# Optimization experiments

Hardware: AMD Instinct MI355X
Metric: run time of the kernel (lower is better)

## Reference

```python
import jax, jax.numpy as jnp
import numpy as np

HEADS = 8
B, N, DIM = 8, 1024, 128  # n must be a perfect square (H=W=32)
LN_EPS = 1e-5


def _region_means(xg):
    """Four-quadrant region means per position via integral image.
    xg: [b,H,W,d] -> [b,H,W,4,d]. For position (h,w) the torch code pools:
      r1 = x[:, :h+1, :w+1], r2 = x[:, :h+1, w:], r3 = x[:, h:, :w+1], r4 = x[:, h:, w:]
    """
    b, H, W, d = xg.shape
    # padded 2D prefix sum: P[:, i, j] = sum over rows<i, cols<j
    P = jnp.pad(jnp.cumsum(jnp.cumsum(xg, axis=1), axis=2),
                ((0, 0), (1, 0), (1, 0), (0, 0)))
    r1 = P[:, 1:, 1:]                                              # sum x[:h+1,:w+1]
    r2 = P[:, 1:, -1:] - P[:, 1:, :-1]                             # sum x[:h+1, w:]
    r3 = P[:, -1:, 1:] - P[:, :-1, 1:]                             # sum x[h:, :w+1]
    r4 = P[:, -1:, -1:] - P[:, :-1, -1:] - P[:, -1:, :-1] + P[:, :-1, :-1]
    ah = jnp.arange(H, dtype=xg.dtype)
    aw = jnp.arange(W, dtype=xg.dtype)
    hp1 = (ah + 1.0)[:, None]   # h+1
    wp1 = (aw + 1.0)[None, :]   # w+1
    hr = (H - ah)[:, None]      # H-h
    wr = (W - aw)[None, :]      # W-w
    c1 = (hp1 * wp1)[None, :, :, None]
    c2 = (hp1 * wr)[None, :, :, None]
    c3 = (hr * wp1)[None, :, :, None]
    c4 = (hr * wr)[None, :, :, None]
    return jnp.stack([r1 / c1, r2 / c2, r3 / c3, r4 / c4], axis=3)


def setup_inputs() -> dict:
    key = jax.random.key(0)
    ks = jax.random.split(key, 10)
    s = 0.02
    return {
        "x": jax.random.normal(ks[0], (B, N, DIM), jnp.float32),
        "ln_g": jnp.ones((DIM,), jnp.float32),
        "ln_b": jnp.zeros((DIM,), jnp.float32),
        "Wqkv": jax.random.normal(ks[1], (DIM, 3 * HEADS * DIM), jnp.float32) * s,
        "bqkv": jax.random.normal(ks[2], (3 * HEADS * DIM,), jnp.float32) * s,
        "Wq": jax.random.normal(ks[3], (DIM, DIM), jnp.float32) * s,
        "Wk": jax.random.normal(ks[4], (DIM, DIM), jnp.float32) * s,
        "Wv": jax.random.normal(ks[5], (DIM, DIM), jnp.float32) * s,
        "Wo": jax.random.normal(ks[6], (DIM, DIM), jnp.float32) * s,
        "bo": jax.random.normal(ks[7], (DIM,), jnp.float32) * s,
        "Wout": jax.random.normal(ks[8], (HEADS * DIM, DIM), jnp.float32) * s,
        "bout": jax.random.normal(ks[9], (DIM,), jnp.float32) * s,
    }


def reference(x, ln_g, ln_b, Wqkv, bqkv, Wq, Wk, Wv, Wo, bo, Wout, bout):
    b, n, dim = x.shape
    H = W = int(n ** 0.5)
    # LayerNorm
    mu = jnp.mean(x, axis=-1, keepdims=True)
    var = jnp.mean(jnp.square(x - mu), axis=-1, keepdims=True)
    xn = (x - mu) * jax.lax.rsqrt(var + LN_EPS) * ln_g + ln_b
    # qkv projection; only q is actually used downstream (k,v chunks are dead)
    qkv = xn @ Wqkv + bqkv
    q = qkv[..., : HEADS * dim].reshape(b, n, HEADS, dim).transpose(0, 2, 1, 3)  # [b,h,n,d]
    # region features, identical across heads -> keep unbroadcast [b,n,4,d]
    regions = _region_means(xn.reshape(b, H, W, dim)).reshape(b, n, 4, dim)
    # RegionAggregator
    qh = q @ Wq                                   # [b,h,n,d]
    k = jnp.einsum('bnrd,de->bnre', regions, Wk)  # [b,n,4,d]
    v = jnp.einsum('bnrd,de->bnre', regions, Wv)
    scale = (dim // HEADS) ** -0.5
    attn = jax.nn.softmax(jnp.einsum('bhnd,bnrd->bhnr', qh, k) * scale, axis=-1)
    agg = jnp.einsum('bhnr,bnrd->bhnd', attn, v)
    out = agg @ Wo + bo                           # [b,h,n,d]
    out = out.transpose(0, 2, 1, 3).reshape(b, n, HEADS * dim)
    return out @ Wout + bout
```

## Files before the change

### kernel.cpp

```cpp
#include <hip/hip_runtime.h>
#include <hip/hip_bf16.h>
#include <stdint.h>

#define HEADS 8
#define NN 1024
#define DIM 128
#define HW 32
#define LN_EPS 1e-5f

typedef __hip_bfloat16 bf16;
typedef __bf16 bf16x8 __attribute__((ext_vector_type(8)));
typedef float floatx4 __attribute__((ext_vector_type(4)));

__device__ __forceinline__ float b2f(bf16 v){ return __bfloat162float(v); }
__device__ __forceinline__ bf16 f2b(float v){ return __float2bfloat16(v); }

__device__ __forceinline__ float ldin(const void* p, size_t i, int f){
    return f ? ((const float*)p)[i] : b2f(((const bf16*)p)[i]);
}
__device__ __forceinline__ float4 ldin4(const void* p, size_t i, int f){
    if (f) return *reinterpret_cast<const float4*>((const float*)p + i);
    ushort4 u = *reinterpret_cast<const ushort4*>((const bf16*)p + i);
    float4 r;
    r.x = b2f(*(bf16*)&u.x); r.y = b2f(*(bf16*)&u.y);
    r.z = b2f(*(bf16*)&u.z); r.w = b2f(*(bf16*)&u.w);
    return r;
}
__device__ __forceinline__ int dtf(const void* g){
    return (((const uint32_t*)g)[0] == 0x3F800000u) ? 1 : 0;
}

__global__ __launch_bounds__(256) void lnscan_kernel(const void* __restrict__ x,
                                                     const void* __restrict__ g,
                                                     const void* __restrict__ bta,
                                                     bf16* __restrict__ xn,
                                                     float* __restrict__ P){
    __shared__ float lnv[32][128];
    int f = dtf(g);
    int b = blockIdx.x >> 5, hh = blockIdx.x & 31;
    int wv = threadIdx.x >> 6, lane = threadIdx.x & 63;
    float gl0 = ldin(g, lane, f),    gl1 = ldin(g, lane+64, f);
    float bl0 = ldin(bta, lane, f),  bl1 = ldin(bta, lane+64, f);
    size_t rowbase = (size_t)b*NN + (size_t)hh*HW;
#pragma unroll
    for (int rnd=0; rnd<8; rnd++){
        int w = rnd*4 + wv;
        size_t base = (rowbase + w)*DIM;
        float v0 = ldin(x, base+lane,    f);
        float v1 = ldin(x, base+lane+64, f);
        float s = v0+v1, ss = v0*v0+v1*v1;
        for (int o=32;o;o>>=1){ s += __shfl_xor(s,o,64); ss += __shfl_xor(ss,o,64); }
        float mu = s * (1.0f/DIM);
        float var = ss * (1.0f/DIM) - mu*mu;
        float rs = rsqrtf(var + LN_EPS);
        float y0 = (v0-mu)*rs*gl0 + bl0;
        float y1 = (v1-mu)*rs*gl1 + bl1;
        xn[base+lane]    = f2b(y0);
        xn[base+lane+64] = f2b(y1);
        lnv[w][lane]    = y0;
        lnv[w][lane+64] = y1;
    }
    __syncthreads();
    if (threadIdx.x < 128){
        int c = threadIdx.x;
        float run = 0.f;
        float* Pr = P + rowbase*DIM + c;
#pragma unroll
        for (int w=0; w<HW; w++){
            run += lnv[w][c];
            Pr[(size_t)w*DIM] = run;
        }
    }
}

__global__ __launch_bounds__(128) void colscan_kernel(float* __restrict__ P){
    int b = blockIdx.x >> 5, w = blockIdx.x & 31, c = threadIdx.x;
    float* Pc = P + ((size_t)(b*NN + w))*DIM + c;
    float run = 0.f;
    for (int h=0; h<HW; h++){
        size_t o = (size_t)h*HW*DIM;
        run += Pc[o]; Pc[o] = run;
    }
}

__global__ __launch_bounds__(256) void prep_kernel(const void* __restrict__ Wqkv,
                                                   const void* __restrict__ bqkv,
                                                   const void* __restrict__ Wq,
                                                   const void* __restrict__ Wk,
                                                   const void* __restrict__ Wv,
                                                   const void* __restrict__ Wo,
                                                   const void* __restrict__ bo,
                                                   const void* __restrict__ Wout,
                                                   const void* __restrict__ ln_g,
                                                   bf16* __restrict__ WhT,
                                                   bf16* __restrict__ WhoT,
                                                   bf16* __restrict__ WkvT,
                                                   float* __restrict__ bq,
                                                   float* __restrict__ bfin_part){
    __shared__ float S1[128][132];
    __shared__ float S2[8][132];
    int f = dtf(ln_g);
    int t = threadIdx.x;
    int blk = blockIdx.x;
    if (blk < 128){
        int h = blk >> 4, dc = blk & 15;
#pragma unroll
        for (int i=0;i<16;i++){
            int idx4 = (t + i*256)*4;
            int k = idx4 >> 7, e = idx4 & 127;
            *reinterpret_cast<float4*>(&S1[k][e]) = ldin4(Wq, idx4, f);
        }
        {
            int idx4 = t*4;
            int dl = idx4 >> 7, k = idx4 & 127;
            *reinterpret_cast<float4*>(&S2[dl][k]) =
                ldin4(Wqkv, (size_t)(dc*8+dl)*3072 + h*128 + k, f);
        }
        __syncthreads();
        int d = t & 7;
        int e0 = (t >> 3) * 4;
        float acc[4] = {0.f,0.f,0.f,0.f};
        for (int k=0;k<128;k++){
            float a = S2[d][k];
            float4 wv = *reinterpret_cast<const float4*>(&S1[k][e0]);
            acc[0] += a*wv.x; acc[1] += a*wv.y; acc[2] += a*wv.z; acc[3] += a*wv.w;
        }
#pragma unroll
        for (int i=0;i<4;i++)
            WhT[(size_t)(h*128 + e0 + i)*128 + dc*8 + d] = f2b(acc[i]);
    } else if (blk < 256){
        int h = (blk-128) >> 4, dc = (blk-128) & 15;
#pragma unroll
        for (int i=0;i<16;i++){
            int idx4 = (t + i*256)*4;
            int k = idx4 >> 7, e = idx4 & 127;
            *reinterpret_cast<float4*>(&S1[k][e]) =
                ldin4(Wout, (size_t)(h*128 + k)*128 + e, f);
        }
        {
            int idx4 = t*4;
            int dl = idx4 >> 7, k = idx4 & 127;
            *reinterpret_cast<float4*>(&S2[dl][k]) =
                ldin4(Wo, (size_t)(dc*8+dl)*128 + k, f);
        }
        __syncthreads();
        int d = t & 7;
        int e0 = (t >> 3) * 4;
        float acc[4] = {0.f,0.f,0.f,0.f};
        for (int k=0;k<128;k++){
            float a = S2[d][k];
            float4 wv = *reinterpret_cast<const float4*>(&S1[k][e0]);
            acc[0] += a*wv.x; acc[1] += a*wv.y; acc[2] += a*wv.z; acc[3] += a*wv.w;
        }
#pragma unroll
        for (int i=0;i<4;i++)
            WhoT[(size_t)(e0 + i)*1024 + h*128 + dc*8 + d] = f2b(acc[i]);
    } else {
        int sub = blk - 256;
        if (sub < 8){
            int h = sub;
            int e = t & 127, kh = t >> 7;
            float s = 0.f;
            for (int k=kh*64; k<kh*64+64; k++)
                s += ldin(bqkv, h*128 + k, f) * ldin(Wq, (size_t)k*128 + e, f);
            S1[kh][e] = s;
            __syncthreads();
            if (t < 128) bq[h*128 + t] = S1[0][t] + S1[1][t];
        } else if (sub < 16){
            int h = sub - 8;
            if (t < 128) S2[0][t] = ldin(bo, t, f);
            __syncthreads();
            int e = t & 127, half = t >> 7;
            float s = 0.f;
            for (int k = half*64; k < half*64 + 64; k++)
                s += S2[0][k] * ldin(Wout, (size_t)(h*128 + k)*128 + e, f);
            S1[half][e] = s;
            __syncthreads();
            if (t < 128) bfin_part[h*128 + t] = S1[0][t] + S1[1][t];
        } else {
            const void* W = (sub == 16) ? Wk : Wv;
            int base = (sub == 16) ? 0 : 128;
#pragma unroll
            for (int i=0;i<16;i++){
                int idx4 = (t + i*256)*4;
                int d = idx4 >> 7, e = idx4 & 127;
                *reinterpret_cast<float4*>(&S1[d][e]) = ldin4(W, idx4, f);
            }
            __syncthreads();
            for (int i=0;i<64;i++){
                int idx = t + i*256; int e = idx >> 7, d = idx & 127;
                WkvT[(size_t)(base + e)*128 + d] = f2b(S1[d][e]);
            }
        }
    }
}

__global__ __launch_bounds__(256) void kvprobs_kernel(const float* __restrict__ P,
                                                      const bf16* __restrict__ WkvT,
                                                      const bf16* __restrict__ WhT,
                                                      const float* __restrict__ bq,
                                                      const bf16* __restrict__ xn,
                                                      bf16* __restrict__ vmat,
                                                      float* __restrict__ probs){
    __shared__ __align__(16) char pool[63488];
    bf16 (*As)[136]     = reinterpret_cast<bf16(*)[136]>(pool);
    bf16 (*kS)[16][136] = reinterpret_cast<bf16(*)[16][136]>(pool);
    bf16 (*Bs)[136]     = reinterpret_cast<bf16(*)[136]>(pool + 17408);
    bf16 (*xnS)[136]    = reinterpret_cast<bf16(*)[136]>(pool + 52224);
    bf16 (*qL)[136]     = reinterpret_cast<bf16(*)[136]>(pool + 56576);
    float* bqS          = reinterpret_cast<float*>(pool + 60928);
    float* logits       = reinterpret_cast<float*>(pool + 61440);

    int t = threadIdx.x;
    int bn0 = blockIdx.x * 16;
    {
        int bn_local = t >> 4;
        int c0 = (t & 15) * 8;
        int bn = bn0 + bn_local;
        int b = bn >> 10, n = bn & 1023;
        int hh = n >> 5, ww = n & 31;
        const float* Pb = P + (size_t)b*NN*DIM;
        auto ld8 = [&](int h, int w, float* o){
            if (h==0 || w==0){
#pragma unroll
                for (int j=0;j<8;j++) o[j] = 0.f;
                return;
            }
            const float* p = Pb + ((size_t)((h-1)*HW + (w-1)))*DIM + c0;
            float4 u = *reinterpret_cast<const float4*>(p);
            float4 v = *reinterpret_cast<const float4*>(p+4);
            o[0]=u.x;o[1]=u.y;o[2]=u.z;o[3]=u.w;o[4]=v.x;o[5]=v.y;o[6]=v.z;o[7]=v.w;
        };
        float f_h1 = (float)(hh+1), f_w1 = (float)(ww+1);
        float f_hr = (float)(HW-hh), f_wr = (float)(HW-ww);
        float a0[8], a1[8];
        ld8(hh+1, ww+1, a0);
#pragma unroll
        for (int j=0;j<8;j++) As[bn_local*4 + 0][c0+j] = f2b(a0[j] / (f_h1*f_w1));
        ld8(hh+1, HW, a0); ld8(hh+1, ww, a1);
#pragma unroll
        for (int j=0;j<8;j++) As[bn_local*4 + 1][c0+j] = f2b((a0[j]-a1[j]) / (f_h1*f_wr));
        ld8(HW, ww+1, a0); ld8(hh, ww+1, a1);
#pragma unroll
        for (int j=0;j<8;j++) As[bn_local*4 + 2][c0+j] = f2b((a0[j]-a1[j]) / (f_hr*f_w1));
        float a2[8], a3[8];
        ld8(HW, HW, a0); ld8(hh, HW, a1); ld8(HW, ww, a2); ld8(hh, ww, a3);
#pragma unroll
        for (int j=0;j<8;j++)
            As[bn_local*4 + 3][c0+j] = f2b((a0[j]-a1[j]-a2[j]+a3[j]) / (f_hr*f_wr));
        *reinterpret_cast<uint4*>(&xnS[t >> 4][(t & 15)*8]) =
            *reinterpret_cast<const uint4*>(&xn[(size_t)(bn0 + (t >> 4))*DIM + (t & 15)*8]);
    }
    int w = t >> 6, lane = t & 63;
    int r = lane & 15, q = lane >> 4;
    floatx4 acc[16];
#pragma unroll
    for (int i=0;i<16;i++) acc[i] = (floatx4){0.f,0.f,0.f,0.f};
    for (int half=0; half<2; half++){
        __syncthreads();
#pragma unroll
        for (int i=0;i<8;i++){
            int id = t + i*256;
            int row = id >> 4, c8 = id & 15;
            *reinterpret_cast<uint4*>(&Bs[row][c8*8]) =
                *reinterpret_cast<const uint4*>(&WkvT[(size_t)(half*128 + row)*128 + c8*8]);
        }
        __syncthreads();
#pragma unroll
        for (int kc=0;kc<4;kc++){
            bf16x8 a = *reinterpret_cast<const bf16x8*>(&As[w*16 + r][kc*32 + q*8]);
#pragma unroll
            for (int nt=0;nt<8;nt++){
                bf16x8 b = *reinterpret_cast<const bf16x8*>(&Bs[nt*16 + r][kc*32 + q*8]);
                acc[half*8+nt] = __builtin_amdgcn_mfma_f32_16x16x32_bf16(a, b, acc[half*8+nt], 0, 0, 0);
            }
        }
    }
#pragma unroll
    for (int nt=0;nt<8;nt++){
#pragma unroll
        for (int i=0;i<4;i++){
            int row = bn0*4 + w*16 + q*4 + i;
            int col = nt*16 + r;
            vmat[(size_t)row*128 + col] = f2b(acc[8+nt][i]);
        }
    }
    __syncthreads();
#pragma unroll
    for (int nt=0;nt<8;nt++){
#pragma unroll
        for (int i=0;i<4;i++){
            int rowg = w*16 + q*4 + i;
            kS[rowg & 3][rowg >> 2][nt*16 + r] = f2b(acc[nt][i]);
        }
    }
    for (int h=0; h<8; h++){
#pragma unroll
        for (int i=0;i<8;i++){
            int id = t + i*256;
            int row = id >> 4, c8 = id & 15;
            *reinterpret_cast<uint4*>(&Bs[row][c8*8]) =
                *reinterpret_cast<const uint4*>(&WhT[(size_t)(h*128 + row)*128 + c8*8]);
        }
        if (t < 128) bqS[t] = bq[h*128 + t];
        __syncthreads();
        floatx4 qa[2];
        qa[0] = (floatx4){0.f,0.f,0.f,0.f};
        qa[1] = (floatx4){0.f,0.f,0.f,0.f};
#pragma unroll
        for (int kc=0;kc<4;kc++){
            bf16x8 a = *reinterpret_cast<const bf16x8*>(&xnS[r][kc*32 + q*8]);
#pragma unroll
            for (int nl=0;nl<2;nl++){
                int nt = w*2 + nl;
                bf16x8 b = *reinterpret_cast<const bf16x8*>(&Bs[nt*16 + r][kc*32 + q*8]);
                qa[nl] = __builtin_amdgcn_mfma_f32_16x16x32_bf16(a, b, qa[nl], 0, 0, 0);
            }
        }
#pragma unroll
        for (int nl=0;nl<2;nl++){
            int col = (w*2 + nl)*16 + r;
            float bb = bqS[col];
#pragma unroll
            for (int i=0;i<4;i++)
                qL[q*4 + i][col] = f2b(qa[nl][i] + bb);
        }
        __syncthreads();
        {
            floatx4 s = (floatx4){0.f,0.f,0.f,0.f};
#pragma unroll
            for (int kc=0;kc<4;kc++){
                bf16x8 a = *reinterpret_cast<const bf16x8*>(&qL[r][kc*32 + q*8]);
                bf16x8 b = *reinterpret_cast<const bf16x8*>(&kS[w][r][kc*32 + q*8]);
                s = __builtin_amdgcn_mfma_f32_16x16x32_bf16(a, b, s, 0, 0, 0);
            }
            if ((r >> 2) == q){
                int i = r & 3;
                float d = (i==0)?s[0]:(i==1)?s[1]:(i==2)?s[2]:s[3];
                logits[(r*8 + h)*4 + w] = d;
            }
        }
    }
    __syncthreads();
    if (t < 128){
        int bn = t >> 3, h = t & 7;
        const float* L = &logits[(bn*8 + h)*4];
        float l0 = L[0]*0.25f, l1 = L[1]*0.25f, l2 = L[2]*0.25f, l3 = L[3]*0.25f;
        float m = fmaxf(fmaxf(l0,l1),fmaxf(l2,l3));
        float e0 = __expf(l0-m), e1=__expf(l1-m), e2=__expf(l2-m), e3=__expf(l3-m);
        float inv = 1.0f/(e0+e1+e2+e3);
        float4 pv = {e0*inv, e1*inv, e2*inv, e3*inv};
        *reinterpret_cast<float4*>(&probs[(size_t)(bn0+bn)*32 + h*4]) = pv;
    }
}

__global__ __launch_bounds__(256) void out_kernel(const float* __restrict__ probs,
                                                  const bf16* __restrict__ vmat,
                                                  const bf16* __restrict__ WhoT,
                                                  const float* __restrict__ bfin_part,
                                                  const void* __restrict__ bout,
                                                  const void* __restrict__ ln_g,
                                                  void* __restrict__ out){
    __shared__ __align__(16) bf16 v_lds[4][32][136];
    __shared__ __align__(16) bf16 Bs[128][136];
    __shared__ __align__(16) float p_lds[32][36];
    int f = dtf(ln_g);
    int t = threadIdx.x;
    int bn0 = blockIdx.x * 32;
#pragma unroll
    for (int i=0;i<8;i++){
        int id = t + i*256;
        int c8 = id & 15, row = (id >> 4) & 31, rg = id >> 9;
        *reinterpret_cast<uint4*>(&v_lds[rg][row][c8*8]) =
            *reinterpret_cast<const uint4*>(&vmat[(size_t)((bn0+row)*4 + rg)*128 + c8*8]);
    }
#pragma unroll
    for (int i=0;i<4;i++){
        int id = t + i*256;
        int row = id >> 5, col = id & 31;
        p_lds[row][col] = probs[(size_t)bn0*32 + id];
    }
    int w = t >> 6, lane = t & 63;
    int r = lane & 15, q = lane >> 4;
    int mh = w & 1, nh = w >> 1;
    int myrow = mh*16 + r;
    floatx4 acc[4];
#pragma unroll
    for (int nt=0;nt<4;nt++) acc[nt] = (floatx4){0.f,0.f,0.f,0.f};

    for (int h=0; h<8; h++){
        __syncthreads();
#pragma unroll
        for (int i=0;i<8;i++){
            int id = t + i*256;
            int row = id >> 4, c8 = id & 15;
            *reinterpret_cast<uint4*>(&Bs[row][c8*8]) =
                *reinterpret_cast<const uint4*>(&WhoT[(size_t)row*1024 + h*128 + c8*8]);
        }
        __syncthreads();
        float4 pv = *reinterpret_cast<const float4*>(&p_lds[myrow][h*4]);
#pragma unroll
        for (int kc=0;kc<4;kc++){
            int c = kc*32 + q*8;
            bf16x8 v0 = *reinterpret_cast<const bf16x8*>(&v_lds[0][myrow][c]);
            bf16x8 v1 = *reinterpret_cast<const bf16x8*>(&v_lds[1][myrow][c]);
            bf16x8 v2 = *reinterpret_cast<const bf16x8*>(&v_lds[2][myrow][c]);
            bf16x8 v3 = *reinterpret_cast<const bf16x8*>(&v_lds[3][myrow][c]);
            bf16x8 a;
#pragma unroll
            for (int j=0;j<8;j++){
                float s = pv.x*(float)v0[j] + pv.y*(float)v1[j]
                        + pv.z*(float)v2[j] + pv.w*(float)v3[j];
                a[j] = (__bf16)s;
            }
#pragma unroll
            for (int nt=0;nt<4;nt++){
                bf16x8 b = *reinterpret_cast<const bf16x8*>(&Bs[nh*64 + nt*16 + r][kc*32 + q*8]);
                acc[nt] = __builtin_amdgcn_mfma_f32_16x16x32_bf16(a, b, acc[nt], 0, 0, 0);
            }
        }
    }
#pragma unroll
    for (int nt=0;nt<4;nt++){
        int col = nh*64 + nt*16 + r;
        float bias = ldin(bout, col, f);
#pragma unroll
        for (int h=0;h<8;h++) bias += bfin_part[h*128 + col];
#pragma unroll
        for (int i=0;i<4;i++){
            int row = bn0 + mh*16 + q*4 + i;
            float v = acc[nt][i] + bias;
            if (f) ((float*)out)[(size_t)row*DIM + col] = v;
            else   ((bf16*)out)[(size_t)row*DIM + col] = f2b(v);
        }
    }
}

extern "C" void kernel_launch(void* const* d_in, const int* in_sizes, int n_in,
                              void* d_out, int out_size, void* d_ws, size_t ws_size,
                              hipStream_t stream){
    const void* x    = d_in[0];
    const void* ln_g = d_in[1];
    const void* ln_b = d_in[2];
    const void* Wqkv = d_in[3];
    const void* bqkv = d_in[4];
    const void* Wq   = d_in[5];
    const void* Wk   = d_in[6];
    const void* Wv   = d_in[7];
    const void* Wo   = d_in[8];
    const void* bo   = d_in[9];
    const void* Wout = d_in[10];
    const void* bout = d_in[11];

    char* ws = (char*)d_ws;
    size_t off = 0;
    auto alloc = [&](size_t bytes)->char*{
        char* p = ws + off; off += (bytes + 255) & ~size_t(255); return p;
    };
    bf16*  WhT   = (bf16*)alloc((size_t)1024*128*2);
    bf16*  WkvT  = (bf16*)alloc((size_t)256*128*2);
    bf16*  WhoT  = (bf16*)alloc((size_t)128*1024*2);
    float* bq    = (float*)alloc(1024*4);
    float* bfin_part = (float*)alloc(8*128*4);
    float* P     = (float*)alloc((size_t)8*NN*DIM*4);
    bf16*  xn    = (bf16*)alloc((size_t)8192*128*2);
    bf16*  vmat  = (bf16*)alloc((size_t)32768*128*2);
    float* probs = (float*)alloc((size_t)8192*32*4);

    prep_kernel<<<274, 256, 0, stream>>>(Wqkv, bqkv, Wq, Wk, Wv, Wo, bo, Wout,
                                         ln_g, WhT, WhoT, WkvT, bq, bfin_part);
    lnscan_kernel<<<256, 256, 0, stream>>>(x, ln_g, ln_b, xn, P);
    colscan_kernel<<<256, 128, 0, stream>>>(P);
    kvprobs_kernel<<<512, 256, 0, stream>>>(P, WkvT, WhT, bq, xn, vmat, probs);
    out_kernel<<<256, 256, 0, stream>>>(probs, vmat, WhoT, bfin_part, bout, ln_g, d_out);
}
```

Measured before the change: 153.5 us.

## Fuse kv/probs and output projection kernels, read weights directly from global

Merges the kvprobs and out kernels into one attention kernel, so the per-position V matrix and softmax probabilities stay in shared memory. This removes the global round-trip through the vmat and probs buffers and one kernel launch. The per-head Wh and Who weight tiles are no longer staged in LDS; MFMA B operands are loaded straight from global/L2, which shrinks LDS use but puts more repeated global loads in the inner loops. Each block now handles 16 rows for the output GEMM instead of 32, so the Who weights are reread twice as often.

```diff
diff --git a/kernel.cpp b/kernel.cpp
--- a/kernel.cpp
+++ b/kernel.cpp
@@ -195,22 +195,27 @@
     }
 }
 
-__global__ __launch_bounds__(256) void kvprobs_kernel(const float* __restrict__ P,
-                                                      const bf16* __restrict__ WkvT,
-                                                      const bf16* __restrict__ WhT,
-                                                      const float* __restrict__ bq,
-                                                      const bf16* __restrict__ xn,
-                                                      bf16* __restrict__ vmat,
-                                                      float* __restrict__ probs){
-    __shared__ __align__(16) char pool[63488];
+__global__ __launch_bounds__(256) void attn_fused_kernel(const float* __restrict__ P,
+                                                         const bf16* __restrict__ WkvT,
+                                                         const bf16* __restrict__ WhT,
+                                                         const bf16* __restrict__ WhoT,
+                                                         const float* __restrict__ bq,
+                                                         const float* __restrict__ bfin_part,
+                                                         const void* __restrict__ bout,
+                                                         const bf16* __restrict__ xn,
+                                                         const void* __restrict__ ln_g,
+                                                         void* __restrict__ out){
+    __shared__ __align__(16) char pool[56576];
     bf16 (*As)[136]     = reinterpret_cast<bf16(*)[136]>(pool);
     bf16 (*kS)[16][136] = reinterpret_cast<bf16(*)[16][136]>(pool);
+    bf16 (*vS)[16][136] = reinterpret_cast<bf16(*)[16][136]>(pool);
     bf16 (*Bs)[136]     = reinterpret_cast<bf16(*)[136]>(pool + 17408);
+    bf16 (*qL)[136]     = reinterpret_cast<bf16(*)[136]>(pool + 17408);
+    float* logits       = reinterpret_cast<float*>(pool + 21760);
+    float4* probsS      = reinterpret_cast<float4*>(pool + 23808);
     bf16 (*xnS)[136]    = reinterpret_cast<bf16(*)[136]>(pool + 52224);
-    bf16 (*qL)[136]     = reinterpret_cast<bf16(*)[136]>(pool + 56576);
-    float* bqS          = reinterpret_cast<float*>(pool + 60928);
-    float* logits       = reinterpret_cast<float*>(pool + 61440);
-
+
+    int f = dtf(ln_g);
     int t = threadIdx.x;
     int bn0 = blockIdx.x * 16;
     {
@@ -276,15 +281,6 @@
             }
         }
     }
-#pragma unroll
-    for (int nt=0;nt<8;nt++){
-#pragma unroll
-        for (int i=0;i<4;i++){
-            int row = bn0*4 + w*16 + q*4 + i;
-            int col = nt*16 + r;
-            vmat[(size_t)row*128 + col] = f2b(acc[8+nt][i]);
-        }
-    }
     __syncthreads();
 #pragma unroll
     for (int nt=0;nt<8;nt++){
@@ -295,15 +291,6 @@
         }
     }
     for (int h=0; h<8; h++){
-#pragma unroll
-        for (int i=0;i<8;i++){
-            int id = t + i*256;
-            int row = id >> 4, c8 = id & 15;
-            *reinterpret_cast<uint4*>(&Bs[row][c8*8]) =
-                *reinterpret_cast<const uint4*>(&WhT[(size_t)(h*128 + row)*128 + c8*8]);
-        }
-        if (t < 128) bqS[t] = bq[h*128 + t];
-        __syncthreads();
         floatx4 qa[2];
         qa[0] = (floatx4){0.f,0.f,0.f,0.f};
         qa[1] = (floatx4){0.f,0.f,0.f,0.f};
@@ -312,15 +299,17 @@
             bf16x8 a = *reinterpret_cast<const bf16x8*>(&xnS[r][kc*32 + q*8]);
 #pragma unroll
             for (int nl=0;nl<2;nl++){
-                int nt = w*2 + nl;
-                bf16x8 b = *reinterpret_cast<const bf16x8*>(&Bs[nt*16 + r][kc*32 + q*8]);
+                int e = (w*2 + nl)*16 + r;
+                bf16x8 b = *reinterpret_cast<const bf16x8*>(
+                    &WhT[((size_t)(h*128 + e))*128 + kc*32 + q*8]);
                 qa[nl] = __builtin_amdgcn_mfma_f32_16x16x32_bf16(a, b, qa[nl], 0, 0, 0);
             }
         }
+        __syncthreads();
 #pragma unroll
         for (int nl=0;nl<2;nl++){
             int col = (w*2 + nl)*16 + r;
-            float bb = bqS[col];
+            float bb = bq[h*128 + col];
 #pragma unroll
             for (int i=0;i<4;i++)
                 qL[q*4 + i][col] = f2b(qa[nl][i] + bb);
@@ -349,63 +338,29 @@
         float m = fmaxf(fmaxf(l0,l1),fmaxf(l2,l3));
         float e0 = __expf(l0-m), e1=__expf(l1-m), e2=__expf(l2-m), e3=__expf(l3-m);
         float inv = 1.0f/(e0+e1+e2+e3);
-        float4 pv = {e0*inv, e1*inv, e2*inv, e3*inv};
-        *reinterpret_cast<float4*>(&probs[(size_t)(bn0+bn)*32 + h*4]) = pv;
-    }
-}
-
-__global__ __launch_bounds__(256) void out_kernel(const float* __restrict__ probs,
-                                                  const bf16* __restrict__ vmat,
-                                                  const bf16* __restrict__ WhoT,
-                                                  const float* __restrict__ bfin_part,
-                                                  const void* __restrict__ bout,
-                                                  const void* __restrict__ ln_g,
-                                                  void* __restrict__ out){
-    __shared__ __align__(16) bf16 v_lds[4][32][136];
-    __shared__ __align__(16) bf16 Bs[128][136];
-    __shared__ __align__(16) float p_lds[32][36];
-    int f = dtf(ln_g);
-    int t = threadIdx.x;
-    int bn0 = blockIdx.x * 32;
-#pragma unroll
-    for (int i=0;i<8;i++){
-        int id = t + i*256;
-        int c8 = id & 15, row = (id >> 4) & 31, rg = id >> 9;
-        *reinterpret_cast<uint4*>(&v_lds[rg][row][c8*8]) =
-            *reinterpret_cast<const uint4*>(&vmat[(size_t)((bn0+row)*4 + rg)*128 + c8*8]);
-    }
-#pragma unroll
-    for (int i=0;i<4;i++){
-        int id = t + i*256;
-        int row = id >> 5, col = id & 31;
-        p_lds[row][col] = probs[(size_t)bn0*32 + id];
-    }
-    int w = t >> 6, lane = t & 63;
-    int r = lane & 15, q = lane >> 4;
-    int mh = w & 1, nh = w >> 1;
-    int myrow = mh*16 + r;
-    floatx4 acc[4];
-#pragma unroll
-    for (int nt=0;nt<4;nt++) acc[nt] = (floatx4){0.f,0.f,0.f,0.f};
-
+        probsS[bn*8 + h] = (float4){e0*inv, e1*inv, e2*inv, e3*inv};
+    }
+#pragma unroll
+    for (int nt=0;nt<8;nt++){
+#pragma unroll
+        for (int i=0;i<4;i++){
+            int rowg = w*16 + q*4 + i;
+            vS[rowg & 3][rowg >> 2][nt*16 + r] = f2b(acc[8+nt][i]);
+        }
+    }
+    __syncthreads();
+    floatx4 oacc[2];
+    oacc[0] = (floatx4){0.f,0.f,0.f,0.f};
+    oacc[1] = (floatx4){0.f,0.f,0.f,0.f};
     for (int h=0; h<8; h++){
-        __syncthreads();
-#pragma unroll
-        for (int i=0;i<8;i++){
-            int id = t + i*256;
-            int row = id >> 4, c8 = id & 15;
-            *reinterpret_cast<uint4*>(&Bs[row][c8*8]) =
-                *reinterpret_cast<const uint4*>(&WhoT[(size_t)row*1024 + h*128 + c8*8]);
-        }
-        __syncthreads();
-        float4 pv = *reinterpret_cast<const float4*>(&p_lds[myrow][h*4]);
+        float4 pv = *reinterpret_cast<const float4*>(&probsS[r*8 + h]);
 #pragma unroll
         for (int kc=0;kc<4;kc++){
             int c = kc*32 + q*8;
-            bf16x8 v0 = *reinterpret_cast<const bf16x8*>(&v_lds[0][myrow][c]);
-            bf16x8 v1 = *reinterpret_cast<const bf16x8*>(&v_lds[1][myrow][c]);
-            bf16x8 v2 = *reinterpret_cast<const bf16x8*>(&v_lds[2][myrow][c]);
-            bf16x8 v3 = *reinterpret_cast<const bf16x8*>(&v_lds[3][myrow][c]);
+            bf16x8 v0 = *reinterpret_cast<const bf16x8*>(&vS[0][r][c]);
+            bf16x8 v1 = *reinterpret_cast<const bf16x8*>(&vS[1][r][c]);
+            bf16x8 v2 = *reinterpret_cast<const bf16x8*>(&vS[2][r][c]);
+            bf16x8 v3 = *reinterpret_cast<const bf16x8*>(&vS[3][r][c]);
             bf16x8 a;
 #pragma unroll
             for (int j=0;j<8;j++){
@@ -414,22 +369,24 @@
                 a[j] = (__bf16)s;
             }
 #pragma unroll
-            for (int nt=0;nt<4;nt++){
-                bf16x8 b = *reinterpret_cast<const bf16x8*>(&Bs[nh*64 + nt*16 + r][kc*32 + q*8]);
-                acc[nt] = __builtin_amdgcn_mfma_f32_16x16x32_bf16(a, b, acc[nt], 0, 0, 0);
-            }
-        }
-    }
-#pragma unroll
-    for (int nt=0;nt<4;nt++){
-        int col = nh*64 + nt*16 + r;
+            for (int nl=0;nl<2;nl++){
+                int e = (w*2 + nl)*16 + r;
+                bf16x8 b = *reinterpret_cast<const bf16x8*>(
+                    &WhoT[(size_t)e*1024 + h*128 + kc*32 + q*8]);
+                oacc[nl] = __builtin_amdgcn_mfma_f32_16x16x32_bf16(a, b, oacc[nl], 0, 0, 0);
+            }
+        }
+    }
+#pragma unroll
+    for (int nl=0;nl<2;nl++){
+        int col = (w*2 + nl)*16 + r;
         float bias = ldin(bout, col, f);
 #pragma unroll
         for (int h=0;h<8;h++) bias += bfin_part[h*128 + col];
 #pragma unroll
         for (int i=0;i<4;i++){
-            int row = bn0 + mh*16 + q*4 + i;
-            float v = acc[nt][i] + bias;
+            int row = bn0 + q*4 + i;
+            float v = oacc[nl][i] + bias;
             if (f) ((float*)out)[(size_t)row*DIM + col] = v;
             else   ((bf16*)out)[(size_t)row*DIM + col] = f2b(v);
         }
@@ -464,13 +421,11 @@
     float* bfin_part = (float*)alloc(8*128*4);
     float* P     = (float*)alloc((size_t)8*NN*DIM*4);
     bf16*  xn    = (bf16*)alloc((size_t)8192*128*2);
-    bf16*  vmat  = (bf16*)alloc((size_t)32768*128*2);
-    float* probs = (float*)alloc((size_t)8192*32*4);
 
     prep_kernel<<<274, 256, 0, stream>>>(Wqkv, bqkv, Wq, Wk, Wv, Wo, bo, Wout,
                                          ln_g, WhT, WhoT, WkvT, bq, bfin_part);
     lnscan_kernel<<<256, 256, 0, stream>>>(x, ln_g, ln_b, xn, P);
     colscan_kernel<<<256, 128, 0, stream>>>(P);
-    kvprobs_kernel<<<512, 256, 0, stream>>>(P, WkvT, WhT, bq, xn, vmat, probs);
-    out_kernel<<<256, 256, 0, stream>>>(probs, vmat, WhoT, bfin_part, bout, ln_g, d_out);
-}
+    attn_fused_kernel<<<512, 256, 0, stream>>>(P, WkvT, WhT, WhoT, bq, bfin_part,
+                                               bout, xn, ln_g, d_out);
+}
```

Result: faster. 147.0 us (-4.2%).
